# Kernel tuning notes

Measured on AMD Instinct MI355X. Metric: run time of the kernel, lower is better.

## Reference

```python
import jax, jax.numpy as jnp
import numpy as np

N_NODES = 100000
N_EDGES = 1600000

def gcn_conv(x, src, dst, W, b, n):
    # symmetric GCN normalization with self-loops already included in src/dst
    deg = jax.ops.segment_sum(jnp.ones_like(src, dtype=x.dtype), dst, num_segments=n)
    dinv = jnp.where(deg > 0, jax.lax.rsqrt(deg), 0.0)
    norm = dinv[src] * dinv[dst]            # [E]
    h = x @ W                                # [n, out]
    msg = h[src] * norm[:, None]             # gather + scale, [E, out]
    out = jax.ops.segment_sum(msg, dst, num_segments=n)  # scatter-add
    return out + b

def setup_inputs() -> dict:
    key = jax.random.key(0)
    k1, k2, k3, k4 = jax.random.split(key, 4)
    x = jax.random.normal(k1, (N_NODES, 768), dtype=jnp.float32)
    edge_index = jax.random.randint(k2, (2, N_EDGES), 0, N_NODES, dtype=jnp.int64)
    W1 = jax.random.normal(k3, (768, 64), dtype=jnp.float32) * (1.0 / np.sqrt(768))
    b1 = jnp.zeros((64,), dtype=jnp.float32)
    W2 = jax.random.normal(k4, (64, 32), dtype=jnp.float32) * (1.0 / np.sqrt(64))
    b2 = jnp.zeros((32,), dtype=jnp.float32)
    return {"x": x, "edge_index": edge_index, "W1": W1, "b1": b1, "W2": W2, "b2": b2}

def reference(x, edge_index, W1, b1, W2, b2):
    n = x.shape[0]
    loop = jnp.arange(n, dtype=edge_index.dtype)
    src = jnp.concatenate([edge_index[0], loop])
    dst = jnp.concatenate([edge_index[1], loop])
    h = jax.nn.relu(gcn_conv(x, src, dst, W1, b1, n))
    # F.dropout with training=False -> identity (eval mode)
    out = gcn_conv(h, src, dst, W2, b2, n)
    return out
```

## Files before the change

### kernel.cpp

```cpp
#include <hip/hip_runtime.h>


constexpr int C1 = 64;
constexpr int C2 = 32;
constexpr int K1 = 768;
constexpr int SCAN_BS = 256;
constexpr int SCAN_ELEMS = 2048;

__global__ void detect_k(const int* __restrict__ ei32, int* flag, int n_words) {
    __shared__ int any_nz;
    if (threadIdx.x == 0) any_nz = 0;
    __syncthreads();
    int w = 2 * threadIdx.x + 1;
    if (w < n_words && ei32[w] != 0) atomicOr(&any_nz, 1);
    __syncthreads();
    if (threadIdx.x == 0) *flag = (any_nz == 0) ? 1 : 0;
}

__device__ __forceinline__ int load_idx(const void* ei, size_t pos, int m64) {
    if (m64) return (int)((const long long*)ei)[pos];
    return ((const int*)ei)[pos];
}

__global__ void zero_k(int* p, int n) {
    int i = blockIdx.x * 256 + threadIdx.x;
    if (i < n) p[i] = 0;
}

__global__ void cnt_k(const void* __restrict__ ei, const int* __restrict__ flag,
                      int* cnt, int E) {
    int e = blockIdx.x * 256 + threadIdx.x;
    if (e >= E) return;
    int m64 = *flag;
    int d = load_idx(ei, (size_t)E + e, m64);
    atomicAdd(&cnt[d], 1);
}

__global__ void dinv_k(const int* __restrict__ cnt, float* dinv, int n) {
    int i = blockIdx.x * 256 + threadIdx.x;
    if (i < n) dinv[i] = rsqrtf(1.0f + (float)cnt[i]);
}

__global__ void scan1_k(const int* __restrict__ cnt, int* partials, int n) {
    __shared__ int s[SCAN_BS];
    int base = blockIdx.x * SCAN_ELEMS;
    int t = threadIdx.x;
    int sum = 0;
    #pragma unroll
    for (int i = 0; i < 8; ++i) {
        int idx = base + t * 8 + i;
        if (idx < n) sum += cnt[idx];
    }
    s[t] = sum;
    __syncthreads();
    for (int off = 128; off > 0; off >>= 1) {
        if (t < off) s[t] += s[t + off];
        __syncthreads();
    }
    if (t == 0) partials[blockIdx.x] = s[0];
}

__global__ void scan2_k(int* partials, int* total_out, int nb) {
    __shared__ int s[256];
    int t = threadIdx.x;
    int v = (t < nb) ? partials[t] : 0;
    s[t] = v;
    __syncthreads();
    for (int off = 1; off < 256; off <<= 1) {
        int add = (t >= off) ? s[t - off] : 0;
        __syncthreads();
        s[t] += add;
        __syncthreads();
    }
    if (t < nb) partials[t] = s[t] - v;
    if (t == 0) *total_out = s[255];
}

__global__ void scan3_k(const int* __restrict__ cnt, const int* __restrict__ partials,
                        int* offsets, int* cursor, int n) {
    __shared__ int s[SCAN_BS];
    int base = blockIdx.x * SCAN_ELEMS;
    int t = threadIdx.x;
    int local[8];
    int sum = 0;
    #pragma unroll
    for (int i = 0; i < 8; ++i) {
        int idx = base + t * 8 + i;
        int v = (idx < n) ? cnt[idx] : 0;
        local[i] = sum;
        sum += v;
    }
    int mine = sum;
    s[t] = sum;
    __syncthreads();
    for (int off = 1; off < 256; off <<= 1) {
        int add = (t >= off) ? s[t - off] : 0;
        __syncthreads();
        s[t] += add;
        __syncthreads();
    }
    int texcl = s[t] - mine;
    int boff = partials[blockIdx.x];
    #pragma unroll
    for (int i = 0; i < 8; ++i) {
        int idx = base + t * 8 + i;
        if (idx < n) {
            int o = boff + texcl + local[i];
            offsets[idx] = o;
            cursor[idx] = o;
        }
    }
}

__global__ void fill_k(const void* __restrict__ ei, const int* __restrict__ flag,
                       int* cursor, int* adj, int E) {
    int e = blockIdx.x * 256 + threadIdx.x;
    if (e >= E) return;
    int m64 = *flag;
    int s = load_idx(ei, e, m64);
    int d = load_idx(ei, (size_t)E + e, m64);
    int pos = atomicAdd(&cursor[d], 1);
    adj[pos] = s;
}

__global__ __launch_bounds__(256) void gemm1_k(const float* __restrict__ x,
                                               const float* __restrict__ W,
                                               const float* __restrict__ dinv,
                                               float* __restrict__ g1, int n) {
    __shared__ float As[32][64];
    __shared__ float Bs[32][64];
    const int tid = threadIdx.x;
    const int block_row = blockIdx.x * 64;
    const int tr = tid >> 4;
    const int tc = tid & 15;

    float acc[4][4] = {};

    for (int k0 = 0; k0 < K1; k0 += 32) {
        #pragma unroll
        for (int i = 0; i < 2; ++i) {
            int f = tid + i * 256;
            int row = f >> 3;
            int k4 = (f & 7) << 2;
            int grow = block_row + row;
            float4 v = make_float4(0.f, 0.f, 0.f, 0.f);
            if (grow < n) v = *(const float4*)(x + (size_t)grow * K1 + k0 + k4);
            As[k4 + 0][row] = v.x; As[k4 + 1][row] = v.y;
            As[k4 + 2][row] = v.z; As[k4 + 3][row] = v.w;
        }
        #pragma unroll
        for (int i = 0; i < 2; ++i) {
            int f = tid + i * 256;
            int kr = f >> 4;
            int c4 = (f & 15) << 2;
            *(float4*)&Bs[kr][c4] = *(const float4*)(W + (size_t)(k0 + kr) * C1 + c4);
        }
        __syncthreads();
        #pragma unroll
        for (int kk = 0; kk < 32; ++kk) {
            float4 a = *(float4*)&As[kk][tr << 2];
            float4 b = *(float4*)&Bs[kk][tc << 2];
            acc[0][0] += a.x * b.x; acc[0][1] += a.x * b.y; acc[0][2] += a.x * b.z; acc[0][3] += a.x * b.w;
            acc[1][0] += a.y * b.x; acc[1][1] += a.y * b.y; acc[1][2] += a.y * b.z; acc[1][3] += a.y * b.w;
            acc[2][0] += a.z * b.x; acc[2][1] += a.z * b.y; acc[2][2] += a.z * b.z; acc[2][3] += a.z * b.w;
            acc[3][0] += a.w * b.x; acc[3][1] += a.w * b.y; acc[3][2] += a.w * b.z; acc[3][3] += a.w * b.w;
        }
        __syncthreads();
    }
    #pragma unroll
    for (int i = 0; i < 4; ++i) {
        int grow = block_row + (tr << 2) + i;
        if (grow < n) {
            float dv = dinv[grow];
            *(float4*)(g1 + (size_t)grow * C1 + (tc << 2)) =
                make_float4(acc[i][0] * dv, acc[i][1] * dv, acc[i][2] * dv, acc[i][3] * dv);
        }
    }
}

__global__ __launch_bounds__(256) void gather1_k(const int* __restrict__ offsets,
                                                 const int* __restrict__ adj,
                                                 const float* __restrict__ dinv,
                                                 const float* __restrict__ g1,
                                                 const float* __restrict__ b1,
                                                 const float* __restrict__ W2,
                                                 float* __restrict__ g2, int n) {
    __shared__ float sW[C1 * C2];
    __shared__ float srow[4][C1];
    const int tid = threadIdx.x;
    for (int i = tid; i < C1 * C2; i += 256) sW[i] = W2[i];

    const int wid = tid >> 6;
    const int c = tid & 63;
    const int v = blockIdx.x * 4 + wid;

    float r = 0.f;
    float dv = 0.f;
    if (v < n) {
        dv = dinv[v];
        int start = offsets[v], end = offsets[v + 1];
        float acc = g1[(size_t)v * C1 + c];
        int j = start;
        for (; j + 4 <= end; j += 4) {
            int s0 = adj[j], s1 = adj[j + 1], s2 = adj[j + 2], s3 = adj[j + 3];
            float a0 = g1[(size_t)s0 * C1 + c];
            float a1 = g1[(size_t)s1 * C1 + c];
            float a2 = g1[(size_t)s2 * C1 + c];
            float a3 = g1[(size_t)s3 * C1 + c];
            acc += (a0 + a1) + (a2 + a3);
        }
        for (; j < end; ++j) acc += g1[(size_t)adj[j] * C1 + c];
        r = fmaxf(b1[c] + dv * acc, 0.f);
    }
    srow[wid][c] = r;
    __syncthreads();

    if (v < n && c < C2) {
        float acc = 0.f;
        #pragma unroll
        for (int k = 0; k < C1; ++k) acc += srow[wid][k] * sW[k * C2 + c];
        g2[(size_t)v * C2 + c] = dv * acc;
    }
}

__global__ __launch_bounds__(256) void gather2_k(const int* __restrict__ offsets,
                                                 const int* __restrict__ adj,
                                                 const float* __restrict__ dinv,
                                                 const float* __restrict__ g2,
                                                 const float* __restrict__ b2,
                                                 float* __restrict__ out, int n) {
    int v = blockIdx.x * 8 + (threadIdx.x >> 5);
    int c = threadIdx.x & 31;
    if (v >= n) return;
    int start = offsets[v], end = offsets[v + 1];
    float acc = g2[(size_t)v * C2 + c];
    int j = start;
    for (; j + 4 <= end; j += 4) {
        int s0 = adj[j], s1 = adj[j + 1], s2 = adj[j + 2], s3 = adj[j + 3];
        float a0 = g2[(size_t)s0 * C2 + c];
        float a1 = g2[(size_t)s1 * C2 + c];
        float a2 = g2[(size_t)s2 * C2 + c];
        float a3 = g2[(size_t)s3 * C2 + c];
        acc += (a0 + a1) + (a2 + a3);
    }
    for (; j < end; ++j) acc += g2[(size_t)adj[j] * C2 + c];
    out[(size_t)v * C2 + c] = b2[c] + dinv[v] * acc;
}

extern "C" void kernel_launch(void* const* d_in, const int* in_sizes, int n_in,
                              void* d_out, int out_size, void* d_ws, size_t ws_size,
                              hipStream_t stream) {
    const float* x  = (const float*)d_in[0];
    const void*  ei = d_in[1];
    const float* W1 = (const float*)d_in[2];
    const float* b1 = (const float*)d_in[3];
    const float* W2 = (const float*)d_in[4];
    const float* b2 = (const float*)d_in[5];
    float* out = (float*)d_out;

    const int n = in_sizes[0] / K1;
    const int E = in_sizes[1] / 2;

    float* ws      = (float*)d_ws;
    int*   flag    = (int*)ws;
    float* dinv    = ws + 16;
    float* g1      = dinv + n;
    float* g2      = g1 + (size_t)n * C1;
    int*   cnt     = (int*)(g2 + (size_t)n * C2);
    int*   offsets = cnt + n;
    int*   cursor  = offsets + n + 1;
    int*   partials= cursor + n;
    int*   adj     = partials + 256;

    const int nb_scan = (n + SCAN_ELEMS - 1) / SCAN_ELEMS;

    detect_k<<<1, 256, 0, stream>>>((const int*)ei, flag, in_sizes[1]);
    zero_k<<<(n + 255) / 256, 256, 0, stream>>>(cnt, n);
    cnt_k<<<(E + 255) / 256, 256, 0, stream>>>(ei, flag, cnt, E);
    dinv_k<<<(n + 255) / 256, 256, 0, stream>>>(cnt, dinv, n);

    gemm1_k<<<(n + 63) / 64, 256, 0, stream>>>(x, W1, dinv, g1, n);

    scan1_k<<<nb_scan, SCAN_BS, 0, stream>>>(cnt, partials, n);
    scan2_k<<<1, 256, 0, stream>>>(partials, offsets + n, nb_scan);
    scan3_k<<<nb_scan, SCAN_BS, 0, stream>>>(cnt, partials, offsets, cursor, n);
    fill_k<<<(E + 255) / 256, 256, 0, stream>>>(ei, flag, cursor, adj, E);

    gather1_k<<<(n + 3) / 4, 256, 0, stream>>>(offsets, adj, dinv, g1, b1, W2, g2, n);
    gather2_k<<<(n + 7) / 8, 256, 0, stream>>>(offsets, adj, dinv, g2, b2, out, n);
}
```

Before: 819.7 us.

## Enlarge GEMM row tile, batch nodes per block in gather1, unroll gathers by 8

The first GEMM now computes 128 rows per block, with 8x4 accumulators per thread and a padded A tile, so fewer blocks reload the W tiles. gather1 handles 32 nodes per block with 8 nodes per wavefront, which amortises loading W2 into shared memory over more nodes and spreads the small 64x32 matmul across all threads. Both gather kernels unroll the neighbour loop to 8 loads to keep more memory requests in flight. The costs are higher register pressure in the GEMM, fewer blocks in gather1, and possible LDS bank conflicts from the scalar strided A reads.

```diff
diff --git a/kernel.cpp b/kernel.cpp
--- a/kernel.cpp
+++ b/kernel.cpp
@@ -6,6 +6,7 @@
 constexpr int K1 = 768;
 constexpr int SCAN_BS = 256;
 constexpr int SCAN_ELEMS = 2048;
+constexpr int G1_NODES = 32;
 
 __global__ void detect_k(const int* __restrict__ ei32, int* flag, int n_words) {
     __shared__ int any_nz;
@@ -127,21 +128,21 @@
                                                const float* __restrict__ W,
                                                const float* __restrict__ dinv,
                                                float* __restrict__ g1, int n) {
-    __shared__ float As[32][64];
+    __shared__ float As[32][129];
     __shared__ float Bs[32][64];
     const int tid = threadIdx.x;
-    const int block_row = blockIdx.x * 64;
+    const int block_row = blockIdx.x * 128;
     const int tr = tid >> 4;
     const int tc = tid & 15;
 
-    float acc[4][4] = {};
+    float acc[8][4] = {};
 
     for (int k0 = 0; k0 < K1; k0 += 32) {
         #pragma unroll
-        for (int i = 0; i < 2; ++i) {
+        for (int i = 0; i < 4; ++i) {
             int f = tid + i * 256;
             int row = f >> 3;
-            int k4 = (f & 7) << 2;
+            int k4  = (f & 7) << 2;
             int grow = block_row + row;
             float4 v = make_float4(0.f, 0.f, 0.f, 0.f);
             if (grow < n) v = *(const float4*)(x + (size_t)grow * K1 + k0 + k4);
@@ -156,20 +157,23 @@
             *(float4*)&Bs[kr][c4] = *(const float4*)(W + (size_t)(k0 + kr) * C1 + c4);
         }
         __syncthreads();
-        #pragma unroll
+        #pragma unroll 8
         for (int kk = 0; kk < 32; ++kk) {
-            float4 a = *(float4*)&As[kk][tr << 2];
             float4 b = *(float4*)&Bs[kk][tc << 2];
-            acc[0][0] += a.x * b.x; acc[0][1] += a.x * b.y; acc[0][2] += a.x * b.z; acc[0][3] += a.x * b.w;
-            acc[1][0] += a.y * b.x; acc[1][1] += a.y * b.y; acc[1][2] += a.y * b.z; acc[1][3] += a.y * b.w;
-            acc[2][0] += a.z * b.x; acc[2][1] += a.z * b.y; acc[2][2] += a.z * b.z; acc[2][3] += a.z * b.w;
-            acc[3][0] += a.w * b.x; acc[3][1] += a.w * b.y; acc[3][2] += a.w * b.z; acc[3][3] += a.w * b.w;
-        }
-        __syncthreads();
-    }
-    #pragma unroll
-    for (int i = 0; i < 4; ++i) {
-        int grow = block_row + (tr << 2) + i;
+            float a[8];
+            #pragma unroll
+            for (int i = 0; i < 8; ++i) a[i] = As[kk][(tr << 3) + i];
+            #pragma unroll
+            for (int i = 0; i < 8; ++i) {
+                acc[i][0] += a[i] * b.x; acc[i][1] += a[i] * b.y;
+                acc[i][2] += a[i] * b.z; acc[i][3] += a[i] * b.w;
+            }
+        }
+        __syncthreads();
+    }
+    #pragma unroll
+    for (int i = 0; i < 8; ++i) {
+        int grow = block_row + (tr << 3) + i;
         if (grow < n) {
             float dv = dinv[grow];
             *(float4*)(g1 + (size_t)grow * C1 + (tc << 2)) =
@@ -186,40 +190,59 @@
                                                  const float* __restrict__ W2,
                                                  float* __restrict__ g2, int n) {
     __shared__ float sW[C1 * C2];
-    __shared__ float srow[4][C1];
+    __shared__ float srow[G1_NODES][C1];
+    __shared__ float sdv[G1_NODES];
     const int tid = threadIdx.x;
-    for (int i = tid; i < C1 * C2; i += 256) sW[i] = W2[i];
+    #pragma unroll
+    for (int i = 0; i < (C1 * C2) / 256; ++i) sW[tid + i * 256] = W2[tid + i * 256];
 
     const int wid = tid >> 6;
     const int c = tid & 63;
-    const int v = blockIdx.x * 4 + wid;
-
-    float r = 0.f;
-    float dv = 0.f;
-    if (v < n) {
-        dv = dinv[v];
-        int start = offsets[v], end = offsets[v + 1];
-        float acc = g1[(size_t)v * C1 + c];
-        int j = start;
-        for (; j + 4 <= end; j += 4) {
-            int s0 = adj[j], s1 = adj[j + 1], s2 = adj[j + 2], s3 = adj[j + 3];
-            float a0 = g1[(size_t)s0 * C1 + c];
-            float a1 = g1[(size_t)s1 * C1 + c];
-            float a2 = g1[(size_t)s2 * C1 + c];
-            float a3 = g1[(size_t)s3 * C1 + c];
-            acc += (a0 + a1) + (a2 + a3);
-        }
-        for (; j < end; ++j) acc += g1[(size_t)adj[j] * C1 + c];
-        r = fmaxf(b1[c] + dv * acc, 0.f);
-    }
-    srow[wid][c] = r;
-    __syncthreads();
-
-    if (v < n && c < C2) {
-        float acc = 0.f;
-        #pragma unroll
-        for (int k = 0; k < C1; ++k) acc += srow[wid][k] * sW[k * C2 + c];
-        g2[(size_t)v * C2 + c] = dv * acc;
+    const int base = blockIdx.x * G1_NODES;
+    const float bc = b1[c];
+
+    #pragma unroll
+    for (int i = 0; i < 8; ++i) {
+        const int slot = wid * 8 + i;
+        const int v = base + slot;
+        float r = 0.f;
+        if (v < n) {
+            float dv = dinv[v];
+            if (c == 0) sdv[slot] = dv;
+            int start = offsets[v], end = offsets[v + 1];
+            float acc = g1[(size_t)v * C1 + c];
+            int j = start;
+            for (; j + 8 <= end; j += 8) {
+                int s0 = adj[j + 0], s1 = adj[j + 1], s2 = adj[j + 2], s3 = adj[j + 3];
+                int s4 = adj[j + 4], s5 = adj[j + 5], s6 = adj[j + 6], s7 = adj[j + 7];
+                float a0 = g1[(size_t)s0 * C1 + c];
+                float a1 = g1[(size_t)s1 * C1 + c];
+                float a2 = g1[(size_t)s2 * C1 + c];
+                float a3 = g1[(size_t)s3 * C1 + c];
+                float a4 = g1[(size_t)s4 * C1 + c];
+                float a5 = g1[(size_t)s5 * C1 + c];
+                float a6 = g1[(size_t)s6 * C1 + c];
+                float a7 = g1[(size_t)s7 * C1 + c];
+                acc += ((a0 + a1) + (a2 + a3)) + ((a4 + a5) + (a6 + a7));
+            }
+            for (; j < end; ++j) acc += g1[(size_t)adj[j] * C1 + c];
+            r = fmaxf(bc + dv * acc, 0.f);
+        }
+        srow[slot][c] = r;
+    }
+    __syncthreads();
+
+    #pragma unroll
+    for (int k = 0; k < 4; ++k) {
+        int idx = tid + k * 256;
+        int node = idx >> 5, ch = idx & 31;
+        int v = base + node;
+        if (v < n) {
+            float acc = 0.f;
+            #pragma unroll
+            for (int kk = 0; kk < C1; ++kk) acc += srow[node][kk] * sW[kk * C2 + ch];
+            g2[(size_t)v * C2 + ch] = sdv[node] * acc;
+        }
     }
 }
 
@@ -235,13 +258,18 @@
     int start = offsets[v], end = offsets[v + 1];
     float acc = g2[(size_t)v * C2 + c];
     int j = start;
-    for (; j + 4 <= end; j += 4) {
-        int s0 = adj[j], s1 = adj[j + 1], s2 = adj[j + 2], s3 = adj[j + 3];
+    for (; j + 8 <= end; j += 8) {
+        int s0 = adj[j + 0], s1 = adj[j + 1], s2 = adj[j + 2], s3 = adj[j + 3];
+        int s4 = adj[j + 4], s5 = adj[j + 5], s6 = adj[j + 6], s7 = adj[j + 7];
         float a0 = g2[(size_t)s0 * C2 + c];
         float a1 = g2[(size_t)s1 * C2 + c];
         float a2 = g2[(size_t)s2 * C2 + c];
         float a3 = g2[(size_t)s3 * C2 + c];
-        acc += (a0 + a1) + (a2 + a3);
+        float a4 = g2[(size_t)s4 * C2 + c];
+        float a5 = g2[(size_t)s5 * C2 + c];
+        float a6 = g2[(size_t)s6 * C2 + c];
+        float a7 = g2[(size_t)s7 * C2 + c];
+        acc += ((a0 + a1) + (a2 + a3)) + ((a4 + a5) + (a6 + a7));
     }
     for (; j < end; ++j) acc += g2[(size_t)adj[j] * C2 + c];
     out[(size_t)v * C2 + c] = b2[c] + dinv[v] * acc;
@@ -279,13 +307,13 @@
     cnt_k<<<(E + 255) / 256, 256, 0, stream>>>(ei, flag, cnt, E);
     dinv_k<<<(n + 255) / 256, 256, 0, stream>>>(cnt, dinv, n);
 
-    gemm1_k<<<(n + 63) / 64, 256, 0, stream>>>(x, W1, dinv, g1, n);
+    gemm1_k<<<(n + 127) / 128, 256, 0, stream>>>(x, W1, dinv, g1, n);
 
     scan1_k<<<nb_scan, SCAN_BS, 0, stream>>>(cnt, partials, n);
     scan2_k<<<1, 256, 0, stream>>>(partials, offsets + n, nb_scan);
     scan3_k<<<nb_scan, SCAN_BS, 0, stream>>>(cnt, partials, offsets, cursor, n);
     fill_k<<<(E + 255) / 256, 256, 0, stream>>>(ei, flag, cursor, adj, E);
 
-    gather1_k<<<(n + 3) / 4, 256, 0, stream>>>(offsets, adj, dinv, g1, b1, W2, g2, n);
+    gather1_k<<<(n + G1_NODES - 1) / G1_NODES, 256, 0, stream>>>(offsets, adj, dinv, g1, b1, W2, g2, n);
     gather2_k<<<(n + 7) / 8, 256, 0, stream>>>(offsets, adj, dinv, g2, b2, out, n);
 }
```

Measured after the change: 832.6 us. Within noise of the previous version (+1.6%).
